# Kernel optimization log

Hardware: AMD Instinct MI355X
Metric: run time of the kernel (lower is better)

## Reference

```python
import jax, jax.numpy as jnp
import numpy as np

N_HEAD, D_MODEL, D_K, D_V = 8, 256, 32, 32


def _patches(x, kernel, pad):
    # x: [B, C, H, W] -> [B, C, kernel*kernel, H, W] (zero-padded local windows, like F.unfold)
    B, C, H, W = x.shape
    p = jax.lax.conv_general_dilated_patches(
        x, (kernel, kernel), (1, 1), [(pad, pad), (pad, pad)],
        dimension_numbers=('NCHW', 'OIHW', 'NCHW'))
    # output channels ordered as (c, kh, kw) -> reshape splits cleanly
    return p.reshape(B, C, kernel * kernel, H, W)


def setup_inputs() -> dict:
    key = jax.random.key(0)
    ks = jax.random.split(key, 7)
    B, H, W = 2, 48, 48
    scale = 0.05
    inp = {
        'q': jax.random.normal(ks[0], (B, D_MODEL, H, W), jnp.float32),
        'k': jax.random.normal(ks[1], (B, D_MODEL, H, W), jnp.float32),
        'v': jax.random.normal(ks[2], (B, D_MODEL, H, W), jnp.float32),
        'Wq': jax.random.normal(ks[3], (N_HEAD * D_K, D_MODEL), jnp.float32) * scale,
        'Wk': jax.random.normal(ks[4], (N_HEAD * D_K, D_MODEL), jnp.float32) * scale,
        'Wv': jax.random.normal(ks[5], (N_HEAD * D_V, D_MODEL), jnp.float32) * scale,
        'Wfc': jax.random.normal(ks[6], (D_MODEL, N_HEAD * D_V), jnp.float32) * scale,
        'kernel': 7,
        'pad': 3,
    }
    return inp


def reference(q, k, v, Wq, Wk, Wv, Wfc, kernel, pad):
    residual = q
    B, _, H, W = q.shape
    kk = kernel * kernel
    proj = lambda x, Wm: jnp.einsum('bchw,oc->bohw', x, Wm)
    # 1x1 conv QKV projections (no bias), split into heads
    qh = proj(q, Wq).reshape(B, N_HEAD, D_K, H, W)
    kp = proj(k, Wk)
    vp = proj(v, Wv)
    # local 'focus' attention: each query attends to its kernel x kernel neighborhood
    kpp = _patches(kp, kernel, pad).reshape(B, N_HEAD, D_K, kk, H, W)
    vpp = _patches(vp, kernel, pad).reshape(B, N_HEAD, D_V, kk, H, W)
    temperature = jnp.asarray(D_K, jnp.float32) ** 0.5
    scores = jnp.einsum('bndhw,bndkhw->bnkhw', qh, kpp) / temperature
    attn = jax.nn.softmax(scores, axis=2)
    out = jnp.einsum('bnkhw,bndkhw->bndhw', attn, vpp).reshape(B, N_HEAD * D_V, H, W)
    out = jnp.einsum('bchw,oc->bohw', out, Wfc)  # fc 1x1 conv
    return out + residual
```

## Files before the change

kernel.cpp:

```cpp
#include <hip/hip_runtime.h>

typedef unsigned int u32;
typedef unsigned short u16;
typedef __attribute__((ext_vector_type(8))) _Float16 f16x8;
typedef __attribute__((ext_vector_type(2))) _Float16 f16x2;
typedef __attribute__((ext_vector_type(4))) float f32x4;

namespace {

constexpr int kH = 48, kW = 48, kHW = kH * kW;
constexpr int kC = 256;
constexpr int kB = 2;
constexpr int kM = kB * kHW;
constexpr int kPH = 54, kPW = 56, kPP = kPH * kPW;
constexpr float kInvTemp = 0.17677669529663687f;

constexpr size_t KPAD_U16 = (size_t)16 * kPP * 32;
constexpr size_t QBF_U16 = (size_t)kM * kC;
constexpr int kZeroTasks = 720 * 16 * 2 * 4;
constexpr int kZeroPerBlk = 54;

__device__ __forceinline__ u32 pack2h(float lo, float hi) {
  return __builtin_bit_cast(u32, __builtin_amdgcn_cvt_pkrtz(lo, hi));
}
__device__ __forceinline__ u16 f2h(float f) {
  return __builtin_bit_cast(u16, (_Float16)f);
}
__device__ __forceinline__ float f4e(const float4 v, int i) {
  return (i == 0) ? v.x : (i == 1) ? v.y : (i == 2) ? v.z : v.w;
}

__global__ __launch_bounds__(256) void gemm_qkv_kernel(
    const float* __restrict__ q, const float* __restrict__ k,
    const float* __restrict__ v, const float* __restrict__ Wq,
    const float* __restrict__ Wk, const float* __restrict__ Wv,
    u16* __restrict__ qbf, u16* __restrict__ kpad, u16* __restrict__ vpad) {
  __shared__ __align__(16) u16 As[32 * 64];
  __shared__ __align__(16) u16 Bs[64 * 64];
  const int t = threadIdx.x;

  {
    const int bid = (blockIdx.z * 4 + blockIdx.y) * 144 + blockIdx.x;
    const int T = bid * kZeroPerBlk + t;
    if (t < kZeroPerBlk && T < kZeroTasks) {
      const int ch = T & 3, rest = T >> 2;
      const int pm = rest / 720, bi = rest - pm * 720;
      int y, x;
      if (bi < 336) {
        const int r = bi / 56, c = bi - (bi / 56) * 56;
        y = (r < 3) ? r : 48 + r;
        x = c;
      } else {
        const int r = (bi - 336) >> 3, c = (bi - 336) & 7;
        y = 3 + r;
        x = (c < 3) ? c : c + 48;
      }
      u16* pb = (pm >= 16) ? vpad : kpad;
      const uint4 zz = {0u, 0u, 0u, 0u};
      *(uint4*)&pb[((size_t)(pm & 15) * kPP + y * kPW + x) * 32 + ch * 8] = zz;
    }
  }

  const int z = blockIdx.z;
  const float* X = (z == 0) ? q : (z == 1) ? k : v;
  const float* Wm = (z == 0) ? Wq : (z == 1) ? Wk : Wv;
  const int m0 = blockIdx.x * 32, n0 = blockIdx.y * 64;
  const int bb = m0 / kHW, p0 = m0 - bb * kHW;
  const int l = t & 63, w = t >> 6, wm = w >> 1, wn = w & 1;
  const int mq = t & 7, kp = t >> 3;

  f32x4 acc[2];
#pragma unroll
  for (int nf = 0; nf < 2; ++nf) acc[nf] = (f32x4){0.f, 0.f, 0.f, 0.f};

  for (int kt = 0; kt < 4; ++kt) {
    const int k0 = kt * 64;
    if (kt) __syncthreads();
    {
      const float* ab =
          X + ((size_t)(bb * kC + k0 + kp * 2)) * kHW + p0 + mq * 4;
      const float4 r0 = *(const float4*)(ab);
      const float4 r1 = *(const float4*)(ab + kHW);
#pragma unroll
      for (int i = 0; i < 4; ++i) {
        const int ml = mq * 4 + i;
        const u32 pk = pack2h(f4e(r0, i), f4e(r1, i));
        const int bo = (kp * 4) ^ ((ml & 7) << 4);
        *(u32*)&As[ml * 64 + (bo >> 1)] = pk;
      }
    }
#pragma unroll
    for (int j = 0; j < 4; ++j) {
      const int task2 = t + j * 256;
      const int rr = task2 >> 4, f4i = task2 & 15;
      const float4 val =
          *(const float4*)&Wm[(size_t)(n0 + rr) * kC + k0 + f4i * 4];
      uint2 pk;
      pk.x = pack2h(val.x, val.y);
      pk.y = pack2h(val.z, val.w);
      const int bo = (f4i * 8) ^ ((rr & 7) << 4);
      *(uint2*)&Bs[rr * 64 + (bo >> 1)] = pk;
    }
    __syncthreads();
#pragma unroll
    for (int ks = 0; ks < 2; ++ks) {
      const int bo = ks * 64 + ((l >> 4) << 4);
      const int rowa = wm * 16 + (l & 15);
      const f16x8 a =
          *(const f16x8*)&As[rowa * 64 + ((bo ^ ((rowa & 7) << 4)) >> 1)];
      f16x8 bfr[2];
#pragma unroll
      for (int nf = 0; nf < 2; ++nf) {
        const int row = wn * 32 + nf * 16 + (l & 15);
        bfr[nf] =
            *(const f16x8*)&Bs[row * 64 + ((bo ^ ((row & 7) << 4)) >> 1)];
      }
#pragma unroll
      for (int nf = 0; nf < 2; ++nf)
        acc[nf] = __builtin_amdgcn_mfma_f32_16x16x32_f16(a, bfr[nf], acc[nf],
                                                         0, 0, 0);
    }
  }

  u16* pd = (z == 1) ? kpad : vpad;
#pragma unroll
  for (int nf = 0; nf < 2; ++nf)
#pragma unroll
    for (int i = 0; i < 4; ++i) {
      const int m = m0 + wm * 16 + ((l >> 4) << 2) + i;
      const int o = n0 + wn * 32 + nf * 16 + (l & 15);
      const float val = acc[nf][i];
      if (z == 0) {
        qbf[(size_t)m * kC + o] = f2h(val);
      } else {
        const int p = m - bb * kHW;
        const int y = p / kW, x = p - (p / kW) * kW;
        pd[((size_t)(bb * 8 + (o >> 5)) * kPP + (y + 3) * kPW + (x + 3)) * 32 +
           (o & 31)] = f2h(val);
      }
    }
}

__global__ __launch_bounds__(256) void attn4_kernel(
    const u16* __restrict__ qbf, const u16* __restrict__ kpad,
    const u16* __restrict__ vpad, u16* __restrict__ att) {
  __shared__ __align__(16) u16 kv_[2 * 100 * 40];
  __shared__ float s_w[16][52];

  const int t = threadIdx.x;
  const int bid = blockIdx.x;
  const int g = bid & 7, i = bid >> 3;
  const int bh = g * 2 + (i >= 144 ? 1 : 0);
  const int tile = (i >= 144) ? i - 144 : i;
  const int tyi = tile / 12, txi = tile - tyi * 12;
  const int y0 = tyi * 4, x0 = txi * 4;
  const int b = bh >> 3, h = bh & 7;
  const int px = t >> 4, sub = t & 15;
  const int py = px >> 2, pxx = px & 3;
  const int gp = (y0 + py) * kW + (x0 + pxx);
  const int hpbase = py * 10 + pxx;

  const size_t plane = (size_t)bh * kPP;
  for (int task = t; task < 800; task += 256) {
    const int mat = task >= 400;
    const int rem = task - mat * 400;
    const int hp = rem >> 2, c8 = rem & 3;
    const int hy = hp / 10, hx = hp - hy * 10;
    const size_t src = (plane + (y0 + hy) * kPW + (x0 + hx)) * 32 + c8 * 8;
    *(uint4*)&kv_[mat * 4000 + hp * 40 + c8 * 8] =
        *(const uint4*)&(mat ? vpad : kpad)[src];
  }
  f16x8 qh[4];
  {
    const size_t qb = ((size_t)(b * kHW + gp)) * kC + h * 32;
    qh[0] = *(const f16x8*)&qbf[qb + 0];
    qh[1] = *(const f16x8*)&qbf[qb + 8];
    qh[2] = *(const f16x8*)&qbf[qb + 16];
    qh[3] = *(const f16x8*)&qbf[qb + 24];
  }
  __syncthreads();

  float sc[4];
  float pm = -1e30f;
#pragma unroll
  for (int nn = 0; nn < 4; ++nn) {
    const int n = nn * 16 + sub;
    float s = -1e30f;
    if (n < 49) {
      const int ky = (n * 147) >> 10, kx = n - ky * 7;
      const u16* kr = &kv_[(hpbase + ky * 10 + kx) * 40];
      float dd[4];
#pragma unroll
      for (int c8 = 0; c8 < 4; ++c8) {
        const f16x8 kk = *(const f16x8*)&kr[c8 * 8];
        float d = 0.f;
#pragma unroll
        for (int j = 0; j < 8; ++j) d += (float)kk[j] * (float)qh[c8][j];
        dd[c8] = d;
      }
      s = ((dd[0] + dd[1]) + (dd[2] + dd[3])) * kInvTemp;
    }
    sc[nn] = s;
    pm = fmaxf(pm, s);
  }
  pm = fmaxf(pm, __shfl_xor(pm, 1));
  pm = fmaxf(pm, __shfl_xor(pm, 2));
  pm = fmaxf(pm, __shfl_xor(pm, 4));
  pm = fmaxf(pm, __shfl_xor(pm, 8));
  float zs = 0.f;
#pragma unroll
  for (int nn = 0; nn < 4; ++nn) {
    const int n = nn * 16 + sub;
    const float e = __expf(sc[nn] - pm);
    zs += e;
    if (n < 49) s_w[px][n] = e;
  }
  zs += __shfl_xor(zs, 1);
  zs += __shfl_xor(zs, 2);
  zs += __shfl_xor(zs, 4);
  zs += __shfl_xor(zs, 8);
  const float rinv = 1.0f / zs;

  float oa0 = 0.f, oa1 = 0.f, ob0 = 0.f, ob1 = 0.f;
#pragma unroll
  for (int n = 0; n < 49; ++n) {
    const int ky = n / 7, kx = n % 7;
    const int hp = hpbase + ky * 10 + kx;
    const float wgt = s_w[px][n];
    const u32 vv = *(const u32*)&kv_[4000 + hp * 40 + sub * 2];
    const f16x2 v2 = __builtin_bit_cast(f16x2, vv);
    if (n & 1) {
      ob0 += wgt * (float)v2[0];
      ob1 += wgt * (float)v2[1];
    } else {
      oa0 += wgt * (float)v2[0];
      oa1 += wgt * (float)v2[1];
    }
  }
  const float o0 = oa0 + ob0, o1 = oa1 + ob1;
  *(u32*)&att[((size_t)(b * kHW + gp)) * kC + h * 32 + sub * 2] =
      pack2h(o0 * rinv, o1 * rinv);
}

__global__ __launch_bounds__(256) void gemm_fc_kernel(
    const u16* __restrict__ att, const float* __restrict__ Wfc,
    const float* __restrict__ Res, float* __restrict__ Out) {
  __shared__ __align__(16) u16 As[32 * 64];
  __shared__ __align__(16) u16 Bs[32 * 64];
  const int t = threadIdx.x;
  const int q0 = blockIdx.x * 32;
  const int o0 = blockIdx.y * 32;
  const int bb = q0 / kHW, p0 = q0 - bb * kHW;
  const int l = t & 63, w = t >> 6, wm = w >> 1, wn = w & 1;

  f32x4 acc = {0.f, 0.f, 0.f, 0.f};

  for (int kt = 0; kt < 4; ++kt) {
    const int k0 = kt * 64;
    if (kt) __syncthreads();
#pragma unroll
    for (int j = 0; j < 2; ++j) {
      const int task = t + j * 256;
      const int rr = task >> 4, f4i = task & 15;
      const float4 val =
          *(const float4*)&Wfc[(size_t)(o0 + rr) * kC + k0 + f4i * 4];
      uint2 pk;
      pk.x = pack2h(val.x, val.y);
      pk.y = pack2h(val.z, val.w);
      const int bo = (f4i * 8) ^ ((rr & 7) << 4);
      *(uint2*)&As[rr * 64 + (bo >> 1)] = pk;
    }
    {
      const int rr = t >> 3, ch = t & 7;
      const uint4 val =
          *(const uint4*)&att[(size_t)(q0 + rr) * kC + k0 + ch * 8];
      const int bo = (ch * 16) ^ ((rr & 7) << 4);
      *(uint4*)&Bs[rr * 64 + (bo >> 1)] = val;
    }
    __syncthreads();
#pragma unroll
    for (int ks = 0; ks < 2; ++ks) {
      const int bo = ks * 64 + ((l >> 4) << 4);
      const int rowa = wm * 16 + (l & 15);
      const f16x8 a =
          *(const f16x8*)&As[rowa * 64 + ((bo ^ ((rowa & 7) << 4)) >> 1)];
      const int rowb = wn * 16 + (l & 15);
      const f16x8 bfr =
          *(const f16x8*)&Bs[rowb * 64 + ((bo ^ ((rowb & 7) << 4)) >> 1)];
      acc = __builtin_amdgcn_mfma_f32_16x16x32_f16(a, bfr, acc, 0, 0, 0);
    }
  }
#pragma unroll
  for (int i = 0; i < 4; ++i) {
    const int o = o0 + wm * 16 + ((l >> 4) << 2) + i;
    const int p = p0 + wn * 16 + (l & 15);
    const size_t addr = ((size_t)(bb * kC + o)) * kHW + p;
    Out[addr] = acc[i] + Res[addr];
  }
}

}

extern "C" void kernel_launch(void* const* d_in, const int* in_sizes, int n_in,
                              void* d_out, int out_size, void* d_ws,
                              size_t ws_size, hipStream_t stream) {
  const float* q = (const float*)d_in[0];
  const float* k = (const float*)d_in[1];
  const float* v = (const float*)d_in[2];
  const float* Wq = (const float*)d_in[3];
  const float* Wk = (const float*)d_in[4];
  const float* Wv = (const float*)d_in[5];
  const float* Wfc = (const float*)d_in[6];
  float* out = (float*)d_out;

  u16* ws16 = (u16*)d_ws;
  u16* kpad = ws16;
  u16* vpad = ws16 + KPAD_U16;
  u16* qbf = ws16 + 2 * KPAD_U16;
  u16* att = qbf + QBF_U16;

  gemm_qkv_kernel<<<dim3(kM / 32, kC / 64, 3), 256, 0, stream>>>(
      q, k, v, Wq, Wk, Wv, qbf, kpad, vpad);

  attn4_kernel<<<dim3(2304), 256, 0, stream>>>(qbf, kpad, vpad, att);

  gemm_fc_kernel<<<dim3(kM / 32, kC / 32), 256, 0, stream>>>(att, Wfc, q,
                                                             out);
}
```

Measured before the change: 36.59 us.

## Pre-convert weights to fp16 once and vectorize attention-value accumulation

```diff
diff --git a/kernel.cpp b/kernel.cpp
--- a/kernel.cpp
+++ b/kernel.cpp
@@ -17,6 +17,8 @@
 
 constexpr size_t KPAD_U16 = (size_t)16 * kPP * 32;
 constexpr size_t QBF_U16 = (size_t)kM * kC;
+constexpr size_t ATT_U16 = (size_t)kM * kC;
+constexpr size_t W16_U16 = (size_t)4 * 65536;
 constexpr int kZeroTasks = 720 * 16 * 2 * 4;
 constexpr int kZeroPerBlk = 54;
 
@@ -30,10 +32,26 @@
   return (i == 0) ? v.x : (i == 1) ? v.y : (i == 2) ? v.z : v.w;
 }
 
+__global__ __launch_bounds__(256) void cvtw_kernel(
+    const float* __restrict__ Wq, const float* __restrict__ Wk,
+    const float* __restrict__ Wv, const float* __restrict__ Wfc,
+    u16* __restrict__ w16) {
+  const int idx = blockIdx.x * 256 + threadIdx.x;
+  const int m = idx >> 13, off = (idx & 8191) * 8;
+  const float* src = (m == 0) ? Wq : (m == 1) ? Wk : (m == 2) ? Wv : Wfc;
+  const float4 a = *(const float4*)&src[off];
+  const float4 b = *(const float4*)&src[off + 4];
+  uint4 pk;
+  pk.x = pack2h(a.x, a.y);
+  pk.y = pack2h(a.z, a.w);
+  pk.z = pack2h(b.x, b.y);
+  pk.w = pack2h(b.z, b.w);
+  *(uint4*)&w16[(size_t)m * 65536 + off] = pk;
+}
+
 __global__ __launch_bounds__(256) void gemm_qkv_kernel(
     const float* __restrict__ q, const float* __restrict__ k,
-    const float* __restrict__ v, const float* __restrict__ Wq,
-    const float* __restrict__ Wk, const float* __restrict__ Wv,
+    const float* __restrict__ v, const u16* __restrict__ w16,
     u16* __restrict__ qbf, u16* __restrict__ kpad, u16* __restrict__ vpad) {
   __shared__ __align__(16) u16 As[32 * 64];
   __shared__ __align__(16) u16 Bs[64 * 64];
@@ -63,7 +81,7 @@
 
   const int z = blockIdx.z;
   const float* X = (z == 0) ? q : (z == 1) ? k : v;
-  const float* Wm = (z == 0) ? Wq : (z == 1) ? Wk : Wv;
+  const u16* Wh = w16 + (size_t)z * 65536;
   const int m0 = blockIdx.x * 32, n0 = blockIdx.y * 64;
   const int bb = m0 / kHW, p0 = m0 - bb * kHW;
   const int l = t & 63, w = t >> 6, wm = w >> 1, wn = w & 1;
@@ -90,16 +108,12 @@
       }
     }
 #pragma unroll
-    for (int j = 0; j < 4; ++j) {
+    for (int j = 0; j < 2; ++j) {
       const int task2 = t + j * 256;
-      const int rr = task2 >> 4, f4i = task2 & 15;
-      const float4 val =
-          *(const float4*)&Wm[(size_t)(n0 + rr) * kC + k0 + f4i * 4];
-      uint2 pk;
-      pk.x = pack2h(val.x, val.y);
-      pk.y = pack2h(val.z, val.w);
-      const int bo = (f4i * 8) ^ ((rr & 7) << 4);
-      *(uint2*)&Bs[rr * 64 + (bo >> 1)] = pk;
+      const int rr = task2 >> 3, ch = task2 & 7;
+      const uint4 val = *(const uint4*)&Wh[(size_t)(n0 + rr) * kC + k0 + ch * 8];
+      const int bo = (ch * 16) ^ ((rr & 7) << 4);
+      *(uint4*)&Bs[rr * 64 + (bo >> 1)] = val;
     }
     __syncthreads();
 #pragma unroll
@@ -221,29 +235,39 @@
   zs += __shfl_xor(zs, 8);
   const float rinv = 1.0f / zs;
 
-  float oa0 = 0.f, oa1 = 0.f, ob0 = 0.f, ob1 = 0.f;
-#pragma unroll
-  for (int n = 0; n < 49; ++n) {
-    const int ky = n / 7, kx = n % 7;
-    const int hp = hpbase + ky * 10 + kx;
-    const float wgt = s_w[px][n];
-    const u32 vv = *(const u32*)&kv_[4000 + hp * 40 + sub * 2];
-    const f16x2 v2 = __builtin_bit_cast(f16x2, vv);
-    if (n & 1) {
-      ob0 += wgt * (float)v2[0];
-      ob1 += wgt * (float)v2[1];
-    } else {
-      oa0 += wgt * (float)v2[0];
-      oa1 += wgt * (float)v2[1];
-    }
-  }
-  const float o0 = oa0 + ob0, o1 = oa1 + ob1;
-  *(u32*)&att[((size_t)(b * kHW + gp)) * kC + h * 32 + sub * 2] =
-      pack2h(o0 * rinv, o1 * rinv);
+  const int ngrp = sub >> 2, cgrp = sub & 3;
+  float of[8];
+#pragma unroll
+  for (int j = 0; j < 8; ++j) of[j] = 0.f;
+#pragma unroll
+  for (int j = 0; j < 13; ++j) {
+    const int n = ngrp + j * 4;
+    if (n < 49) {
+      const int ky = n / 7, kx = n - (n / 7) * 7;
+      const int hp = hpbase + ky * 10 + kx;
+      const float wgt = s_w[px][n];
+      const f16x8 vv = *(const f16x8*)&kv_[4000 + hp * 40 + cgrp * 8];
+#pragma unroll
+      for (int c = 0; c < 8; ++c) of[c] += wgt * (float)vv[c];
+    }
+  }
+#pragma unroll
+  for (int c = 0; c < 8; ++c) {
+    of[c] += __shfl_xor(of[c], 4);
+    of[c] += __shfl_xor(of[c], 8);
+  }
+  if (ngrp == 0) {
+    uint4 outv;
+    outv.x = pack2h(of[0] * rinv, of[1] * rinv);
+    outv.y = pack2h(of[2] * rinv, of[3] * rinv);
+    outv.z = pack2h(of[4] * rinv, of[5] * rinv);
+    outv.w = pack2h(of[6] * rinv, of[7] * rinv);
+    *(uint4*)&att[((size_t)(b * kHW + gp)) * kC + h * 32 + cgrp * 8] = outv;
+  }
 }
 
 __global__ __launch_bounds__(256) void gemm_fc_kernel(
-    const u16* __restrict__ att, const float* __restrict__ Wfc,
+    const u16* __restrict__ att, const u16* __restrict__ wfch,
     const float* __restrict__ Res, float* __restrict__ Out) {
   __shared__ __align__(16) u16 As[32 * 64];
   __shared__ __align__(16) u16 Bs[32 * 64];
@@ -258,17 +282,12 @@
   for (int kt = 0; kt < 4; ++kt) {
     const int k0 = kt * 64;
     if (kt) __syncthreads();
-#pragma unroll
-    for (int j = 0; j < 2; ++j) {
-      const int task = t + j * 256;
-      const int rr = task >> 4, f4i = task & 15;
-      const float4 val =
-          *(const float4*)&Wfc[(size_t)(o0 + rr) * kC + k0 + f4i * 4];
-      uint2 pk;
-      pk.x = pack2h(val.x, val.y);
-      pk.y = pack2h(val.z, val.w);
-      const int bo = (f4i * 8) ^ ((rr & 7) << 4);
-      *(uint2*)&As[rr * 64 + (bo >> 1)] = pk;
+    {
+      const int rr = t >> 3, ch = t & 7;
+      const uint4 val =
+          *(const uint4*)&wfch[(size_t)(o0 + rr) * kC + k0 + ch * 8];
+      const int bo = (ch * 16) ^ ((rr & 7) << 4);
+      *(uint4*)&As[rr * 64 + (bo >> 1)] = val;
     }
     {
       const int rr = t >> 3, ch = t & 7;
@@ -318,12 +337,15 @@
   u16* vpad = ws16 + KPAD_U16;
   u16* qbf = ws16 + 2 * KPAD_U16;
   u16* att = qbf + QBF_U16;
+  u16* w16 = att + ATT_U16;
+
+  cvtw_kernel<<<dim3(128), 256, 0, stream>>>(Wq, Wk, Wv, Wfc, w16);
 
   gemm_qkv_kernel<<<dim3(kM / 32, kC / 64, 3), 256, 0, stream>>>(
-      q, k, v, Wq, Wk, Wv, qbf, kpad, vpad);
+      q, k, v, w16, qbf, kpad, vpad);
 
   attn4_kernel<<<dim3(2304), 256, 0, stream>>>(qbf, kpad, vpad, att);
 
-  gemm_fc_kernel<<<dim3(kM / 32, kC / 32), 256, 0, stream>>>(att, Wfc, q,
-                                                             out);
-}
+  gemm_fc_kernel<<<dim3(kM / 32, kC / 32), 256, 0, stream>>>(
+      att, w16 + (size_t)3 * 65536, q, out);
+}
```

Measured after the change: 38.23 us. +4.5%, slower.
